# Performance work log

Hardware: AMD Instinct MI355X
Metric: run time of the kernel (lower is better)

The kernel has to match this reference:

```python
import jax, jax.numpy as jnp
import numpy as np

S_DIM, A_DIM, H_DIM = 256, 18, 256
E, NS, B = 5, 10, 4096  # ensemble, MC samples, batch


def setup_inputs() -> dict:
    key = jax.random.key(0)
    ks = iter(jax.random.split(key, 40))
    def kaiming(k, shape):
        return jax.random.normal(k, shape, jnp.float32) * np.float32(np.sqrt(2.0 / shape[-1]))
    inp = {
        "state": jax.random.normal(next(ks), (B, S_DIM), jnp.float32),
        "num_samples": NS,
    }
    dims = [(H_DIM, S_DIM), (H_DIM, H_DIM), (A_DIM, H_DIM)]
    for i, (o, ii) in enumerate(dims):
        inp[f"w_mu{i}"] = kaiming(next(ks), (E, o, ii))
        inp[f"w_rho{i}"] = jnp.full((E, o, ii), -3.0, jnp.float32)
        inp[f"b_mu{i}"] = jnp.zeros((E, o), jnp.float32)
        inp[f"b_rho{i}"] = jnp.full((E, o), -3.0, jnp.float32)
        inp[f"w_eps{i}"] = jax.random.normal(next(ks), (E, NS, o, ii), jnp.float32)
        inp[f"b_eps{i}"] = jax.random.normal(next(ks), (E, NS, o), jnp.float32)
    # uncertainty head: Linear(2A->H), ReLU, Linear(H->A), Softplus
    inp["uh_w1"] = kaiming(next(ks), (H_DIM, 2 * A_DIM))
    inp["uh_b1"] = jnp.zeros((H_DIM,), jnp.float32)
    inp["uh_w2"] = kaiming(next(ks), (A_DIM, H_DIM))
    inp["uh_b2"] = jnp.zeros((A_DIM,), jnp.float32)
    # risk head: Linear(3A->H), ReLU, Linear(H->1)
    inp["rh_w1"] = kaiming(next(ks), (H_DIM, 3 * A_DIM))
    inp["rh_b1"] = jnp.zeros((H_DIM,), jnp.float32)
    inp["rh_w2"] = kaiming(next(ks), (1, H_DIM))
    inp["rh_b2"] = jnp.zeros((1,), jnp.float32)
    return inp


def _kl(mu, sigma):
    # KL(N(mu, sigma) || N(0, 1)) summed over param dims -> per-ensemble [E]
    kl = -jnp.log(sigma) + (sigma ** 2 + mu ** 2) * 0.5 - 0.5
    return jnp.sum(kl, axis=tuple(range(1, mu.ndim)))


def _bayes(x, wmu, wrho, bmu, brho, weps, beps):
    # x: [E,S,B,in]; wmu: [E,out,in]; weps: [E,S,out,in]
    wsig = jax.nn.softplus(wrho)
    bsig = jax.nn.softplus(brho)
    w = wmu[:, None] + wsig[:, None] * weps        # [E,S,out,in]
    b = bmu[:, None] + bsig[:, None] * beps        # [E,S,out]
    y = jnp.einsum('esbi,esoi->esbo', x, w) + b[:, :, None, :]
    kl = _kl(wmu, wsig) + _kl(bmu, bsig)           # [E] (same for all MC samples)
    return y, kl


def reference(state, num_samples,
              w_mu0, w_rho0, b_mu0, b_rho0, w_eps0, b_eps0,
              w_mu1, w_rho1, b_mu1, b_rho1, w_eps1, b_eps1,
              w_mu2, w_rho2, b_mu2, b_rho2, w_eps2, b_eps2,
              uh_w1, uh_b1, uh_w2, uh_b2,
              rh_w1, rh_b1, rh_w2, rh_b2):
    e, ns = w_eps0.shape[0], w_eps0.shape[1]
    x = jnp.broadcast_to(state, (e, ns) + state.shape)          # [E,S,B,in]
    x, kl0 = _bayes(x, w_mu0, w_rho0, b_mu0, b_rho0, w_eps0, b_eps0)
    x = jax.nn.relu(x)  # dropout = identity (eval)
    x, kl1 = _bayes(x, w_mu1, w_rho1, b_mu1, b_rho1, w_eps1, b_eps1)
    x = jax.nn.relu(x)
    x, kl2 = _bayes(x, w_mu2, w_rho2, b_mu2, b_rho2, w_eps2, b_eps2)
    net_out = x.mean(axis=1)                                     # [E,B,A]
    q_mean = net_out.mean(axis=0)                                # [B,A]
    q_var = jnp.var(net_out, axis=0, ddof=1)                     # unbiased, as torch .var
    epistemic = q_var
    u_in = jnp.concatenate([q_mean, q_var], axis=-1)             # [B,2A]
    h = jax.nn.relu(u_in @ uh_w1.T + uh_b1)
    aleatoric = jax.nn.softplus(h @ uh_w2.T + uh_b2)             # [B,A]
    total_unc = epistemic + aleatoric
    r_in = jnp.concatenate([q_mean, epistemic, aleatoric], axis=-1)  # [B,3A]
    risk = jax.nn.relu(r_in @ rh_w1.T + rh_b1) @ rh_w2.T + rh_b2     # [B,1]
    s = 2.0 * jnp.sqrt(total_unc)
    lcb, ucb = q_mean - s, q_mean + s
    # total_kl = sum_e ns*kl_e ; divided by (E*num_samples) -> mean over ensemble
    kl_div = jnp.sum(kl0 + kl1 + kl2) / e
    return (q_mean, epistemic, aleatoric, total_unc, lcb, ucb, risk, kl_div)
```

## Files before the change

### kernel.cpp

```cpp
#include <hip/hip_runtime.h>
#include <hip/hip_bf16.h>


typedef __bf16 bf16x8 __attribute__((ext_vector_type(8)));
typedef float f32x4 __attribute__((ext_vector_type(4)));
typedef float f32x16 __attribute__((ext_vector_type(16)));
typedef unsigned short u16x4 __attribute__((ext_vector_type(4)));
typedef unsigned short u16x8 __attribute__((ext_vector_type(8)));

__device__ __forceinline__ unsigned short f2bf(float f) {
  unsigned int u = __builtin_bit_cast(unsigned int, f);
  u += 0x7fffu + ((u >> 16) & 1u);
  return (unsigned short)(u >> 16);
}

__device__ __forceinline__ float softplus_f(float x) {
  return (x > 20.f) ? x : __logf(1.f + __expf(x));
}

__device__ __forceinline__ float klterm(float m, float sg) {
  return -__logf(sg) + (sg * sg + m * m) * 0.5f - 0.5f;
}

__device__ __forceinline__ f32x16 mfma32(bf16x8 a, bf16x8 b, f32x16 c) {
  return __builtin_amdgcn_mfma_f32_32x32x16_bf16(a, b, c, 0, 0, 0);
}

template <int O>
__device__ __forceinline__ float wpanel_body(
    int p, int t, const float* __restrict__ wmu, const float* __restrict__ wrho,
    const float* __restrict__ weps, char* __restrict__ wf,
    char* __restrict__ lb) {
  int es = (O == 256) ? (p >> 3) : p;
  int osub = (O == 256) ? (p & 7) : 0;
  int e = es / 10, s = es - e * 10;
  float kl = 0.f;
  int i = (4 * t) & 255;
  int kt2 = i >> 4, byo = (i & 7) * 2, hi32 = 32 * ((i >> 3) & 1);
#pragma unroll
  for (int j = 0; j < 8; ++j) {
    int o = j * 4 + (t >> 6);
    int og = osub * 32 + o;
    float v[4];
    if (O == 256 || og < O) {
      size_t base = ((size_t)(e * O + og)) * 256 + i;
      f32x4 m4 = *(const f32x4*)(wmu + base);
      f32x4 r4 = *(const f32x4*)(wrho + base);
      f32x4 e4 = *(const f32x4*)(weps + ((size_t)((e * 10 + s) * O + og)) * 256 + i);
#pragma unroll
      for (int c = 0; c < 4; ++c) {
        float m = m4[c];
        float sg = softplus_f(r4[c]);
        v[c] = m + sg * e4[c];
        if (s == 0) kl += klterm(m, sg);
      }
    } else {
#pragma unroll
      for (int c = 0; c < 4; ++c) v[c] = 0.f;
    }
    u16x4 pk = {f2bf(v[0]), f2bf(v[1]), f2bf(v[2]), f2bf(v[3])};
    *(u16x4*)(lb + kt2 * 1024 + (o + hi32) * 16 + byo) = pk;
  }
  __syncthreads();
  char* dst = wf + (size_t)p * 16384;
#pragma unroll
  for (int j = 0; j < 4; ++j) {
    int idx = j * 256 + t;
    *(u16x8*)(dst + idx * 16) = *(const u16x8*)(lb + idx * 16);
  }
  return kl;
}

__device__ __forceinline__ void scvt_body(int gid, const float* __restrict__ s,
                                          unsigned short* __restrict__ d) {
  const f32x4* p = (const f32x4*)(s + (size_t)gid * 8);
  f32x4 x0 = p[0], x1 = p[1];
  u16x8 v = {f2bf(x0.x), f2bf(x0.y), f2bf(x0.z), f2bf(x0.w),
             f2bf(x1.x), f2bf(x1.y), f2bf(x1.z), f2bf(x1.w)};
  *(u16x8*)(d + (size_t)gid * 8) = v;
}

__global__ __launch_bounds__(256) void prep_kernel(
    const float* __restrict__ state, unsigned short* __restrict__ stateb,
    const float* __restrict__ wmu0, const float* __restrict__ wrho0,
    const float* __restrict__ weps0, char* __restrict__ W0f,
    const float* __restrict__ wmu1, const float* __restrict__ wrho1,
    const float* __restrict__ weps1, char* __restrict__ W1f,
    const float* __restrict__ wmu2, const float* __restrict__ wrho2,
    const float* __restrict__ weps2, char* __restrict__ W2f,
    const float* __restrict__ bmu0, const float* __restrict__ brho0,
    const float* __restrict__ beps0, const float* __restrict__ bmu1,
    const float* __restrict__ brho1, const float* __restrict__ beps1,
    const float* __restrict__ bmu2, const float* __restrict__ brho2,
    const float* __restrict__ beps2, float* __restrict__ bias0,
    float* __restrict__ bias1, float* __restrict__ bias2,
    float* __restrict__ partials) {
  __shared__ char lb[16384];
  int bid = blockIdx.x, t = threadIdx.x;
  float kl = 0.f;
  if (bid < 512) {
    scvt_body(bid * 256 + t, state, stateb);
  } else if (bid < 912) {
    kl = wpanel_body<256>(bid - 512, t, wmu0, wrho0, weps0, W0f, lb);
  } else if (bid < 1312) {
    kl = wpanel_body<256>(bid - 912, t, wmu1, wrho1, weps1, W1f, lb);
  } else if (bid < 1362) {
    kl = wpanel_body<18>(bid - 1312, t, wmu2, wrho2, weps2, W2f, lb);
  } else {
    int gid = (bid - 1362) * 256 + t;
    if (gid < 12800) {
      int es = gid >> 8, o = gid & 255, e = es / 10, s = es - e * 10;
      float m = bmu0[e * 256 + o];
      float sg = softplus_f(brho0[e * 256 + o]);
      bias0[gid] = m + sg * beps0[(e * 10 + s) * 256 + o];
      if (s == 0) kl = klterm(m, sg);
    } else if (gid < 25600) {
      int id = gid - 12800;
      int es = id >> 8, o = id & 255, e = es / 10, s = es - e * 10;
      float m = bmu1[e * 256 + o];
      float sg = softplus_f(brho1[e * 256 + o]);
      bias1[id] = m + sg * beps1[(e * 10 + s) * 256 + o];
      if (s == 0) kl = klterm(m, sg);
    } else if (gid < 27200) {
      int id = gid - 25600;
      int es = id >> 5, o = id & 31, e = es / 10, s = es - e * 10;
      if (o < 18) {
        float m = bmu2[e * 18 + o];
        float sg = softplus_f(brho2[e * 18 + o]);
        bias2[id] = m + sg * beps2[(e * 10 + s) * 18 + o];
        if (s == 0) kl = klterm(m, sg);
      } else {
        bias2[id] = 0.f;
      }
    }
  }
#pragma unroll
  for (int m = 32; m >= 1; m >>= 1) kl += __shfl_xor(kl, m);
  __shared__ float wsum[4];
  if ((t & 63) == 0) wsum[t >> 6] = kl;
  __syncthreads();
  if (t == 0) partials[bid] = wsum[0] + wsum[1] + wsum[2] + wsum[3];
}

__device__ __forceinline__ void mlp_layer32o(const char* __restrict__ wA,
                                             const float* __restrict__ bias_es,
                                             int og, char* __restrict__ buf,
                                             int lane) {
  const char* ap = wA + (size_t)og * 16384;
  const char* b0p = buf;
  const char* b1p = buf + 16384;
  int lo = lane * 16;
  f32x16 acc0, acc1;
#pragma unroll
  for (int c = 0; c < 16; ++c) { acc0[c] = 0.f; acc1[c] = 0.f; }

  bf16x8 afr[5], bf0[3], bf1[3];
#pragma unroll
  for (int i = 0; i < 4; ++i) afr[i] = *(const bf16x8*)(ap + i * 1024 + lo);
#pragma unroll
  for (int i = 0; i < 3; ++i) {
    bf0[i] = *(const bf16x8*)(b0p + i * 1024 + lo);
    bf1[i] = *(const bf16x8*)(b1p + i * 1024 + lo);
  }
#pragma unroll
  for (int kt = 0; kt < 16; ++kt) {
    if (kt + 4 < 16) afr[(kt + 4) % 5] = *(const bf16x8*)(ap + (kt + 4) * 1024 + lo);
    if (kt + 3 < 16) {
      bf0[(kt + 3) % 3] = *(const bf16x8*)(b0p + (kt + 3) * 1024 + lo);
      bf1[(kt + 3) % 3] = *(const bf16x8*)(b1p + (kt + 3) * 1024 + lo);
    }
    __builtin_amdgcn_s_setprio(1);
    acc0 = mfma32(afr[kt % 5], bf0[kt % 3], acc0);
    acc1 = mfma32(afr[kt % 5], bf1[kt % 3], acc1);
    __builtin_amdgcn_s_setprio(0);
  }
  __syncthreads();

  int hi = lane >> 5, bcol = lane & 15 | (lane & 31);
  bcol = lane & 31;
  auto epi = [&](const f32x16& A, int j) {
    int obt = og * 32;
    char* fb = buf + (size_t)(j * 16) * 1024;
#pragma unroll
    for (int q = 0; q < 4; ++q) {
      int o0 = obt + 8 * q + 4 * hi;
      f32x4 bv = *(const f32x4*)(bias_es + o0);
      float v0 = fmaxf(A[4 * q + 0] + bv.x, 0.f);
      float v1 = fmaxf(A[4 * q + 1] + bv.y, 0.f);
      float v2 = fmaxf(A[4 * q + 2] + bv.z, 0.f);
      float v3 = fmaxf(A[4 * q + 3] + bv.w, 0.f);
      u16x4 pk = {f2bf(v0), f2bf(v1), f2bf(v2), f2bf(v3)};
      int kt2t = o0 >> 4;
      *(u16x4*)(fb + kt2t * 1024 + (bcol + 32 * (q & 1)) * 16 + 8 * hi) = pk;
    }
  };
  epi(acc0, 0);
  epi(acc1, 1);
  __syncthreads();
}

__global__ __launch_bounds__(512, 4) void mlp_fused(
    const unsigned short* __restrict__ stateb, const char* __restrict__ W0f,
    const char* __restrict__ W1f, const char* __restrict__ W2f,
    const float* __restrict__ bias0, const float* __restrict__ bias1,
    const float* __restrict__ bias2, float* __restrict__ y2) {
  __shared__ char lds[40960];
  char* buf = lds;
  float* scratch = (float*)(lds + 32768);
  int tid = threadIdx.x, w = tid >> 6, lane = tid & 63;
  int lo = lane * 16;

  int bid = blockIdx.x;
  int lin = (bid & 7) * 400 + (bid >> 3);
  int es = lin >> 6, b0 = (lin & 63) * 64;

#pragma unroll
  for (int it = 0; it < 4; ++it) {
    int F = it * 8 + w, bt = F >> 4, kt2 = F & 15;
    const unsigned short* src =
        stateb + (size_t)(b0 + bt * 32 + (lane & 31)) * 256 + kt2 * 16 + (lane >> 5) * 8;
    *(u16x8*)(buf + F * 1024 + lo) = *(const u16x8*)src;
  }
  __syncthreads();

  mlp_layer32o(W0f + (size_t)es * 131072, bias0 + es * 256, w, buf, lane);
  mlp_layer32o(W1f + (size_t)es * 131072, bias1 + es * 256, w, buf, lane);

  int bt2 = w & 1, kh = (w >> 1) & 1;
  f32x16 acc2;
#pragma unroll
  for (int c = 0; c < 16; ++c) acc2[c] = 0.f;
  if (w < 4) {
    const char* b2k = buf + (size_t)bt2 * 16384 + kh * 8192;
    const char* w2p = W2f + (size_t)es * 16384 + kh * 8192;
#pragma unroll
    for (int k = 0; k < 8; ++k) {
      bf16x8 a = *(const bf16x8*)(w2p + k * 1024 + lo);
      bf16x8 bb = *(const bf16x8*)(b2k + k * 1024 + lo);
      acc2 = mfma32(a, bb, acc2);
    }
    if (kh == 1) {
#pragma unroll
      for (int q = 0; q < 4; ++q) {
        f32x4 v = {acc2[4 * q], acc2[4 * q + 1], acc2[4 * q + 2], acc2[4 * q + 3]};
        *(f32x4*)(scratch + (size_t)((bt2 * 4 + q) * 64 + lane) * 4) = v;
      }
    }
  }
  __syncthreads();
  if (w < 4 && kh == 0) {
    int hi = lane >> 5, bcol = lane & 31;
    int b_idx = b0 + bt2 * 32 + bcol;
    float* yp = y2 + ((size_t)es * 4096 + b_idx) * 20;
    float s[16];
#pragma unroll
    for (int q = 0; q < 4; ++q) {
      f32x4 p = *(const f32x4*)(scratch + (size_t)((bt2 * 4 + q) * 64 + lane) * 4);
      f32x4 bv = *(const f32x4*)(bias2 + es * 32 + 8 * q + 4 * hi);
      s[4 * q + 0] = acc2[4 * q + 0] + p.x + bv.x;
      s[4 * q + 1] = acc2[4 * q + 1] + p.y + bv.y;
      s[4 * q + 2] = acc2[4 * q + 2] + p.z + bv.z;
      s[4 * q + 3] = acc2[4 * q + 3] + p.w + bv.w;
    }
    if (hi == 0) {
      f32x4 v0 = {s[0], s[1], s[2], s[3]};
      f32x4 v1 = {s[4], s[5], s[6], s[7]};
      float2 v2 = {s[8], s[9]};
      *(f32x4*)(yp) = v0;
      *(f32x4*)(yp + 8) = v1;
      *(float2*)(yp + 16) = v2;
    } else {
      f32x4 v0 = {s[0], s[1], s[2], s[3]};
      f32x4 v1 = {s[4], s[5], s[6], s[7]};
      *(f32x4*)(yp + 4) = v0;
      *(f32x4*)(yp + 12) = v1;
    }
  }
}

__global__ __launch_bounds__(256) void heads_kernel(
    const float* __restrict__ y2, const float* __restrict__ partials,
    const float* __restrict__ uh_w1, const float* __restrict__ uh_b1,
    const float* __restrict__ uh_w2, const float* __restrict__ uh_b2,
    const float* __restrict__ rh_w1, const float* __restrict__ rh_b1,
    const float* __restrict__ rh_w2, const float* __restrict__ rh_b2,
    float* __restrict__ out) {
  int bid = blockIdx.x, t = threadIdx.x;
  if (bid == 512) {
    if (t < 64) {
      float acc = 0.f;
      for (int i = t; i < 1469; i += 64) acc += partials[i];
#pragma unroll
      for (int m = 32; m >= 1; m >>= 1) acc += __shfl_xor(acc, m);
      if (t == 0) out[446464] = acc * 0.2f;
    }
    return;
  }
  int b0 = bid * 8;

  __shared__ float ysh[8][1004];
  __shared__ float qsE[8][90];
  __shared__ float rin[8][56];
  __shared__ float h[8][260];

  for (int i = t; i < 2000; i += 256) {
    int r = i / 250, c = i - r * 250;
    int es_t = c / 5, part = c - es_t * 5;
    *(f32x4*)(&ysh[r][c * 4]) =
        *(const f32x4*)(y2 + ((size_t)es_t * 4096 + b0 + r) * 20 + part * 4);
  }
  __syncthreads();

  for (int i = t; i < 720; i += 256) {
    int r = i / 90, ae = i - r * 90;
    int a = ae / 5, e = ae - a * 5;
    float v = 0.f;
#pragma unroll
    for (int s = 0; s < 10; ++s) v += ysh[r][(e * 10 + s) * 20 + a];
    qsE[r][ae] = v * 0.1f;
  }
  __syncthreads();

  if (t < 144) {
    int r = t / 18, a = t - (t / 18) * 18;
    float qs = 0.f, qq = 0.f;
#pragma unroll
    for (int e = 0; e < 5; ++e) {
      float v = qsE[r][a * 5 + e];
      qs += v;
      qq += v * v;
    }
    float mean = qs * 0.2f;
    float var = fmaxf((qq - 5.f * mean * mean) * 0.25f, 0.f);
    rin[r][a] = mean;
    rin[r][18 + a] = var;
    out[(b0 + r) * 18 + a] = mean;
    out[73728 + (b0 + r) * 18 + a] = var;
  }
  __syncthreads();

  {
    f32x4 wv[9];
    const f32x4* wr = (const f32x4*)(uh_w1 + t * 36);
#pragma unroll
    for (int j = 0; j < 9; ++j) wv[j] = wr[j];
    float bb = uh_b1[t];
#pragma unroll
    for (int r = 0; r < 8; ++r) {
      float acc = bb;
#pragma unroll
      for (int j = 0; j < 9; ++j) {
        acc += wv[j].x * rin[r][j * 4] + wv[j].y * rin[r][j * 4 + 1] +
               wv[j].z * rin[r][j * 4 + 2] + wv[j].w * rin[r][j * 4 + 3];
      }
      h[r][t] = fmaxf(acc, 0.f);
    }
  }
  __syncthreads();

  if (t < 144) {
    int r = t / 18, a = t - (t / 18) * 18;
    float p = 0.f;
    const f32x4* w2r = (const f32x4*)(uh_w2 + a * 256);
#pragma unroll
    for (int j = 0; j < 64; ++j) {
      f32x4 wv = w2r[j];
      f32x4 hv = *(const f32x4*)(&h[r][j * 4]);
      p += wv.x * hv.x + wv.y * hv.y + wv.z * hv.z + wv.w * hv.w;
    }
    float alea = softplus_f(p + uh_b2[a]);
    float qm = rin[r][a], epi = rin[r][18 + a];
    float tu = epi + alea;
    float s2 = 2.f * sqrtf(tu);
    int b = b0 + r;
    out[2 * 73728 + b * 18 + a] = alea;
    out[3 * 73728 + b * 18 + a] = tu;
    out[4 * 73728 + b * 18 + a] = qm - s2;
    out[5 * 73728 + b * 18 + a] = qm + s2;
    rin[r][36 + a] = alea;
  }
  __syncthreads();

  {
    float w1v[54];
    const float2* wr2 = (const float2*)(rh_w1 + t * 54);
#pragma unroll
    for (int j = 0; j < 27; ++j) {
      float2 wv = wr2[j];
      w1v[j * 2] = wv.x;
      w1v[j * 2 + 1] = wv.y;
    }
    float bb = rh_b1[t];
#pragma unroll
    for (int r = 0; r < 8; ++r) {
      float acc = bb;
#pragma unroll
      for (int j = 0; j < 54; ++j) acc += w1v[j] * rin[r][j];
      h[r][t] = fmaxf(acc, 0.f);
    }
  }
  __syncthreads();

  if (t < 8) {
    float p = 0.f;
    const f32x4* w2r = (const f32x4*)(rh_w2);
#pragma unroll
    for (int j = 0; j < 64; ++j) {
      f32x4 wv = w2r[j];
      f32x4 hv = *(const f32x4*)(&h[t][j * 4]);
      p += wv.x * hv.x + wv.y * hv.y + wv.z * hv.z + wv.w * hv.w;
    }
    out[6 * 73728 + b0 + t] = p + rh_b2[0];
  }
}

extern "C" void kernel_launch(void* const* d_in, const int* in_sizes, int n_in,
                              void* d_out, int out_size, void* d_ws, size_t ws_size,
                              hipStream_t stream) {
  const float* state = (const float*)d_in[0];
  const float* w_mu0 = (const float*)d_in[2];
  const float* w_rho0 = (const float*)d_in[3];
  const float* b_mu0 = (const float*)d_in[4];
  const float* b_rho0 = (const float*)d_in[5];
  const float* w_eps0 = (const float*)d_in[6];
  const float* b_eps0 = (const float*)d_in[7];
  const float* w_mu1 = (const float*)d_in[8];
  const float* w_rho1 = (const float*)d_in[9];
  const float* b_mu1 = (const float*)d_in[10];
  const float* b_rho1 = (const float*)d_in[11];
  const float* w_eps1 = (const float*)d_in[12];
  const float* b_eps1 = (const float*)d_in[13];
  const float* w_mu2 = (const float*)d_in[14];
  const float* w_rho2 = (const float*)d_in[15];
  const float* b_mu2 = (const float*)d_in[16];
  const float* b_rho2 = (const float*)d_in[17];
  const float* w_eps2 = (const float*)d_in[18];
  const float* b_eps2 = (const float*)d_in[19];
  const float* uh_w1 = (const float*)d_in[20];
  const float* uh_b1 = (const float*)d_in[21];
  const float* uh_w2 = (const float*)d_in[22];
  const float* uh_b2 = (const float*)d_in[23];
  const float* rh_w1 = (const float*)d_in[24];
  const float* rh_b1 = (const float*)d_in[25];
  const float* rh_w2 = (const float*)d_in[26];
  const float* rh_b2 = (const float*)d_in[27];
  float* out = (float*)d_out;

  char* ws = (char*)d_ws;
  unsigned short* stateb = (unsigned short*)ws;
  char* W0f = ws + 2097152;
  char* W1f = W0f + 6553600;
  char* W2f = W1f + 6553600;
  float* bias0 = (float*)(W2f + 819200);
  float* bias1 = bias0 + 12800;
  float* bias2 = bias1 + 12800;
  float* y2 = bias2 + 1600;
  float* klpart = y2 + (size_t)50 * 4096 * 20;

  prep_kernel<<<1469, 256, 0, stream>>>(
      state, stateb, w_mu0, w_rho0, w_eps0, W0f, w_mu1, w_rho1, w_eps1, W1f,
      w_mu2, w_rho2, w_eps2, W2f, b_mu0, b_rho0, b_eps0, b_mu1, b_rho1, b_eps1,
      b_mu2, b_rho2, b_eps2, bias0, bias1, bias2, klpart);
  mlp_fused<<<3200, 512, 0, stream>>>(stateb, W0f, W1f, W2f, bias0, bias1,
                                      bias2, y2);
  heads_kernel<<<513, 256, 0, stream>>>(y2, klpart, uh_w1, uh_b1, uh_w2, uh_b2,
                                        rh_w1, rh_b1, rh_w2, rh_b2, out);
}
```

Baseline: 113.0 us.

## Stage weight K-slices into LDS asynchronously with double buffering in fused MLP

The fused MLP kernel now runs 4 waves per block instead of 8. Each wave computes a 64x64 output tile with four accumulators. Weight K-slices are streamed from global memory into a double-buffered LDS region using global_load_lds, overlapped with the MFMAs. The first slice of the next layer is prefetched during the epilogue. The prep kernel writes layers 0/1 in a K-major layout to support these contiguous 8KB slice copies. This trades per-wave direct global weight loads for shared LDS staging, adding a barrier every K step and a larger LDS footprint per block.

```diff
diff --git a/kernel.cpp b/kernel.cpp
--- a/kernel.cpp
+++ b/kernel.cpp
@@ -24,6 +24,20 @@
 
 __device__ __forceinline__ f32x16 mfma32(bf16x8 a, bf16x8 b, f32x16 c) {
   return __builtin_amdgcn_mfma_f32_32x32x16_bf16(a, b, c, 0, 0, 0);
+}
+
+__device__ __forceinline__ void async16(void* l, const void* g) {
+  __builtin_amdgcn_global_load_lds(
+      (const __attribute__((address_space(1))) unsigned int*)g,
+      (__attribute__((address_space(3))) unsigned int*)l, 16, 0, 0);
+}
+
+__device__ __forceinline__ void stage8k(const char* __restrict__ g,
+                                        char* __restrict__ l, int w, int lane) {
+  const char* gp = g + w * 2048 + lane * 16;
+  char* lp = l + w * 2048;
+  async16(lp, gp);
+  async16(lp + 1024, gp + 1024);
 }
 
 template <int O>
@@ -62,11 +76,21 @@
     *(u16x4*)(lb + kt2 * 1024 + (o + hi32) * 16 + byo) = pk;
   }
   __syncthreads();
-  char* dst = wf + (size_t)p * 16384;
-#pragma unroll
-  for (int j = 0; j < 4; ++j) {
-    int idx = j * 256 + t;
-    *(u16x8*)(dst + idx * 16) = *(const u16x8*)(lb + idx * 16);
+  if (O == 256) {
+    char* base = wf + (size_t)es * 131072 + (size_t)osub * 1024;
+#pragma unroll
+    for (int j = 0; j < 4; ++j) {
+      int idx = j * 256 + t;
+      int k2 = idx >> 6, u = idx & 63;
+      *(u16x8*)(base + k2 * 8192 + u * 16) = *(const u16x8*)(lb + idx * 16);
+    }
+  } else {
+    char* dst = wf + (size_t)p * 16384;
+#pragma unroll
+    for (int j = 0; j < 4; ++j) {
+      int idx = j * 256 + t;
+      *(u16x8*)(dst + idx * 16) = *(const u16x8*)(lb + idx * 16);
+    }
   }
   return kl;
 }
@@ -142,45 +166,48 @@
   if (t == 0) partials[bid] = wsum[0] + wsum[1] + wsum[2] + wsum[3];
 }
 
-__device__ __forceinline__ void mlp_layer32o(const char* __restrict__ wA,
-                                             const float* __restrict__ bias_es,
-                                             int og, char* __restrict__ buf,
-                                             int lane) {
-  const char* ap = wA + (size_t)og * 16384;
-  const char* b0p = buf;
-  const char* b1p = buf + 16384;
+template <bool PREF_NEXT>
+__device__ __forceinline__ void run_layer(const char* __restrict__ wsrc,
+                                          const char* __restrict__ next_src,
+                                          const float* __restrict__ bias_es,
+                                          char* __restrict__ bact,
+                                          char* __restrict__ adb, int w,
+                                          int lane) {
   int lo = lane * 16;
-  f32x16 acc0, acc1;
-#pragma unroll
-  for (int c = 0; c < 16; ++c) { acc0[c] = 0.f; acc1[c] = 0.f; }
-
-  bf16x8 afr[5], bf0[3], bf1[3];
-#pragma unroll
-  for (int i = 0; i < 4; ++i) afr[i] = *(const bf16x8*)(ap + i * 1024 + lo);
-#pragma unroll
-  for (int i = 0; i < 3; ++i) {
-    bf0[i] = *(const bf16x8*)(b0p + i * 1024 + lo);
-    bf1[i] = *(const bf16x8*)(b1p + i * 1024 + lo);
-  }
-#pragma unroll
-  for (int kt = 0; kt < 16; ++kt) {
-    if (kt + 4 < 16) afr[(kt + 4) % 5] = *(const bf16x8*)(ap + (kt + 4) * 1024 + lo);
-    if (kt + 3 < 16) {
-      bf0[(kt + 3) % 3] = *(const bf16x8*)(b0p + (kt + 3) * 1024 + lo);
-      bf1[(kt + 3) % 3] = *(const bf16x8*)(b1p + (kt + 3) * 1024 + lo);
-    }
+  f32x16 acc00, acc01, acc10, acc11;
+#pragma unroll
+  for (int c = 0; c < 16; ++c) {
+    acc00[c] = 0.f; acc01[c] = 0.f; acc10[c] = 0.f; acc11[c] = 0.f;
+  }
+#pragma unroll
+  for (int c = 0; c < 16; ++c) {
+    asm volatile("s_waitcnt vmcnt(0)" ::: "memory");
+    __builtin_amdgcn_s_barrier();
+    asm volatile("" ::: "memory");
+    if (c < 15)
+      stage8k(wsrc + (size_t)(c + 1) * 8192, adb + ((c + 1) & 1) * 8192, w, lane);
+    const char* ab = adb + (c & 1) * 8192 + lo;
+    bf16x8 a0 = *(const bf16x8*)(ab + (2 * w) * 1024);
+    bf16x8 a1 = *(const bf16x8*)(ab + (2 * w + 1) * 1024);
+    bf16x8 b0 = *(const bf16x8*)(bact + c * 1024 + lo);
+    bf16x8 b1 = *(const bf16x8*)(bact + (16 + c) * 1024 + lo);
     __builtin_amdgcn_s_setprio(1);
-    acc0 = mfma32(afr[kt % 5], bf0[kt % 3], acc0);
-    acc1 = mfma32(afr[kt % 5], bf1[kt % 3], acc1);
+    acc00 = mfma32(a0, b0, acc00);
+    acc01 = mfma32(a0, b1, acc01);
+    acc10 = mfma32(a1, b0, acc10);
+    acc11 = mfma32(a1, b1, acc11);
     __builtin_amdgcn_s_setprio(0);
   }
-  __syncthreads();
-
-  int hi = lane >> 5, bcol = lane & 15 | (lane & 31);
-  bcol = lane & 31;
-  auto epi = [&](const f32x16& A, int j) {
-    int obt = og * 32;
-    char* fb = buf + (size_t)(j * 16) * 1024;
+  asm volatile("" ::: "memory");
+  __builtin_amdgcn_s_barrier();
+  asm volatile("" ::: "memory");
+  if (PREF_NEXT)
+    stage8k(next_src, adb, w, lane);
+
+  int hi = lane >> 5, bcol = lane & 31;
+  auto epi = [&](const f32x16& A, int i, int j) {
+    int obt = w * 64 + i * 32;
+    char* fb = bact + (size_t)(j * 16) * 1024;
 #pragma unroll
     for (int q = 0; q < 4; ++q) {
       int o0 = obt + 8 * q + 4 * hi;
@@ -194,18 +221,23 @@
       *(u16x4*)(fb + kt2t * 1024 + (bcol + 32 * (q & 1)) * 16 + 8 * hi) = pk;
     }
   };
-  epi(acc0, 0);
-  epi(acc1, 1);
-  __syncthreads();
-}
-
-__global__ __launch_bounds__(512, 4) void mlp_fused(
+  epi(acc00, 0, 0);
+  epi(acc01, 0, 1);
+  epi(acc10, 1, 0);
+  epi(acc11, 1, 1);
+  asm volatile("s_waitcnt lgkmcnt(0)" ::: "memory");
+  __builtin_amdgcn_s_barrier();
+  asm volatile("" ::: "memory");
+}
+
+__global__ __launch_bounds__(256, 3) void mlp_fused(
     const unsigned short* __restrict__ stateb, const char* __restrict__ W0f,
     const char* __restrict__ W1f, const char* __restrict__ W2f,
     const float* __restrict__ bias0, const float* __restrict__ bias1,
     const float* __restrict__ bias2, float* __restrict__ y2) {
-  __shared__ char lds[40960];
-  char* buf = lds;
+  __shared__ char lds[49152];
+  char* bact = lds;
+  char* adb = lds + 32768;
   float* scratch = (float*)(lds + 32768);
   int tid = threadIdx.x, w = tid >> 6, lane = tid & 63;
   int lo = lane * 16;
@@ -214,41 +246,44 @@
   int lin = (bid & 7) * 400 + (bid >> 3);
   int es = lin >> 6, b0 = (lin & 63) * 64;
 
-#pragma unroll
-  for (int it = 0; it < 4; ++it) {
-    int F = it * 8 + w, bt = F >> 4, kt2 = F & 15;
+  const char* w0src = W0f + (size_t)es * 131072;
+  const char* w1src = W1f + (size_t)es * 131072;
+
+  stage8k(w0src, adb, w, lane);
+
+#pragma unroll
+  for (int it = 0; it < 8; ++it) {
+    int F = it * 4 + w, bt = F >> 4, kt2 = F & 15;
     const unsigned short* src =
         stateb + (size_t)(b0 + bt * 32 + (lane & 31)) * 256 + kt2 * 16 + (lane >> 5) * 8;
-    *(u16x8*)(buf + F * 1024 + lo) = *(const u16x8*)src;
-  }
-  __syncthreads();
-
-  mlp_layer32o(W0f + (size_t)es * 131072, bias0 + es * 256, w, buf, lane);
-  mlp_layer32o(W1f + (size_t)es * 131072, bias1 + es * 256, w, buf, lane);
-
-  int bt2 = w & 1, kh = (w >> 1) & 1;
+    *(u16x8*)(bact + F * 1024 + lo) = *(const u16x8*)src;
+  }
+  __syncthreads();
+
+  run_layer<true>(w0src, w1src, bias0 + es * 256, bact, adb, w, lane);
+  run_layer<false>(w1src, nullptr, bias1 + es * 256, bact, adb, w, lane);
+
+  int bt2 = w & 1, kh = w >> 1;
   f32x16 acc2;
 #pragma unroll
   for (int c = 0; c < 16; ++c) acc2[c] = 0.f;
-  if (w < 4) {
-    const char* b2k = buf + (size_t)bt2 * 16384 + kh * 8192;
-    const char* w2p = W2f + (size_t)es * 16384 + kh * 8192;
-#pragma unroll
-    for (int k = 0; k < 8; ++k) {
-      bf16x8 a = *(const bf16x8*)(w2p + k * 1024 + lo);
-      bf16x8 bb = *(const bf16x8*)(b2k + k * 1024 + lo);
-      acc2 = mfma32(a, bb, acc2);
-    }
-    if (kh == 1) {
-#pragma unroll
-      for (int q = 0; q < 4; ++q) {
-        f32x4 v = {acc2[4 * q], acc2[4 * q + 1], acc2[4 * q + 2], acc2[4 * q + 3]};
-        *(f32x4*)(scratch + (size_t)((bt2 * 4 + q) * 64 + lane) * 4) = v;
-      }
-    }
-  }
-  __syncthreads();
-  if (w < 4 && kh == 0) {
+  const char* b2k = bact + (size_t)bt2 * 16384 + kh * 8192;
+  const char* w2p = W2f + (size_t)es * 16384 + kh * 8192;
+#pragma unroll
+  for (int k = 0; k < 8; ++k) {
+    bf16x8 a = *(const bf16x8*)(w2p + k * 1024 + lo);
+    bf16x8 bb = *(const bf16x8*)(b2k + k * 1024 + lo);
+    acc2 = mfma32(a, bb, acc2);
+  }
+  if (kh == 1) {
+#pragma unroll
+    for (int q = 0; q < 4; ++q) {
+      f32x4 v = {acc2[4 * q], acc2[4 * q + 1], acc2[4 * q + 2], acc2[4 * q + 3]};
+      *(f32x4*)(scratch + (size_t)((bt2 * 4 + q) * 64 + lane) * 4) = v;
+    }
+  }
+  __syncthreads();
+  if (kh == 0) {
     int hi = lane >> 5, bcol = lane & 31;
     int b_idx = b0 + bt2 * 32 + bcol;
     float* yp = y2 + ((size_t)es * 4096 + b_idx) * 20;
@@ -461,7 +496,7 @@
       state, stateb, w_mu0, w_rho0, w_eps0, W0f, w_mu1, w_rho1, w_eps1, W1f,
       w_mu2, w_rho2, w_eps2, W2f, b_mu0, b_rho0, b_eps0, b_mu1, b_rho1, b_eps1,
       b_mu2, b_rho2, b_eps2, bias0, bias1, bias2, klpart);
-  mlp_fused<<<3200, 512, 0, stream>>>(stateb, W0f, W1f, W2f, bias0, bias1,
+  mlp_fused<<<3200, 256, 0, stream>>>(stateb, W0f, W1f, W2f, bias0, bias1,
                                       bias2, y2);
   heads_kernel<<<513, 256, 0, stream>>>(y2, klpart, uh_w1, uh_b1, uh_w2, uh_b2,
                                         rh_w1, rh_b1, rh_w2, rh_b2, out);
```

Result: slower. 121.4 us (+7.4%).
